# Kernel optimization log

Measured on AMD Instinct MI355X. Metric: run time of the kernel, lower is better.

Reference implementation:

```python
import jax, jax.numpy as jnp
import numpy as np

B, A, N_IN = 128, 96, 128  # molecules, atoms per molecule, feature dim
H1, H2 = 64, 1             # gated-equivariant MLP widths: 128 -> 64 -> 1


def _mlp(x, W1, b1, W2, b2):
    return jax.nn.silu(x @ W1 + b1) @ W2 + b2


def _gated_block(s, v, Wmix, Ws1, bs1, Ws2, bs2, n_out, sact):
    # s: [N, n_sin], v: [N, 3, n_vin]
    vmix = jnp.einsum('ndi,io->ndo', v, Wmix)          # [N, 3, 2*n_out]
    vV, vW = vmix[..., :n_out], vmix[..., n_out:]
    vVn = jnp.linalg.norm(vV, axis=-2)                 # [N, n_out]
    x = _mlp(jnp.concatenate([s, vVn], axis=-1), Ws1, bs1, Ws2, bs2)
    s_out, gate = x[..., :n_out], x[..., n_out:]
    v_out = gate[:, None, :] * vW                      # [N, 3, n_out]
    if sact:
        s_out = jax.nn.silu(s_out)
    return s_out, v_out


def setup_inputs():
    key = jax.random.key(0)
    ks = iter(jax.random.split(key, 40))
    def W(shape):
        return jax.random.normal(next(ks), shape, jnp.float32) / np.sqrt(shape[0]).astype(np.float32)
    N = B * A
    return dict(
        positions=jax.random.normal(next(ks), (N, 3), jnp.float32) * 3.0,
        scalar_rep=jax.random.normal(next(ks), (N, N_IN), jnp.float32),
        vector_rep=jax.random.normal(next(ks), (N, 3, N_IN), jnp.float32),
        mix_W1=W((N_IN, 2 * H1)),
        sc1_W1=W((N_IN + H1, N_IN)), sc1_b1=jnp.zeros((N_IN,), jnp.float32),
        sc1_W2=W((N_IN, 2 * H1)), sc1_b2=jnp.zeros((2 * H1,), jnp.float32),
        mix_W2=W((H1, 2 * H2)),
        sc2_W1=W((H1 + H2, H1)), sc2_b1=jnp.zeros((H1,), jnp.float32),
        sc2_W2=W((H1, 2 * H2)), sc2_b2=jnp.zeros((2 * H2,), jnp.float32),
        vv_W1=W((9, 30)), vv_b1=jnp.zeros((30,), jnp.float32), vv_W2=W((30, 9)), vv_b2=jnp.zeros((9,), jnp.float32),
        vr_W1=W((9, 30)), vr_b1=jnp.zeros((30,), jnp.float32), vr_W2=W((30, 9)), vr_b2=jnp.zeros((9,), jnp.float32),
        s_W1=W((2, 30)), s_b1=jnp.zeros((30,), jnp.float32), s_W2=W((30, 9)), s_b2=jnp.zeros((9,), jnp.float32),
        h_W1=W((9, 30)), h_b1=jnp.zeros((30,), jnp.float32), h_W2=W((30, 9)), h_b2=jnp.zeros((9,), jnp.float32),
        n_atoms=jnp.full((B,), A, dtype=jnp.int32),
    )


def reference(positions, scalar_rep, vector_rep,
              mix_W1, sc1_W1, sc1_b1, sc1_W2, sc1_b2,
              mix_W2, sc2_W1, sc2_b1, sc2_W2, sc2_b2,
              vv_W1, vv_b1, vv_W2, vv_b2,
              vr_W1, vr_b1, vr_W2, vr_b2,
              s_W1, s_b1, s_W2, s_b2,
              h_W1, h_b1, h_W2, h_b2, n_atoms):
    # outnet: gated equivariant MLP 128 -> 64 (silu on scalars) -> 1 (no sact)
    s, v = _gated_block(scalar_rep, vector_rep, mix_W1, sc1_W1, sc1_b1, sc1_W2, sc1_b2, H1, True)
    s, v = _gated_block(s, v, mix_W2, sc2_W1, sc2_b1, sc2_W2, sc2_b2, H2, False)
    l0 = s[:, 0].reshape(B, A)          # [B, A]
    l1 = v[:, :, 0].reshape(B, A, 3)    # [B, A, 3]
    pos = positions.reshape(B, A, 3)
    # per-pair outer products, flattened 3x3 -> 9 (row-major k,l as in torch view)
    vv = jnp.einsum('bik,bjl->bijkl', l1, l1).reshape(B, A, A, 9)
    vr = jnp.einsum('bik,bjl->bijkl', l1, pos).reshape(B, A, A, 9)
    vv = _mlp(vv, vv_W1, vv_b1, vv_W2, vv_b2)
    vr = _mlp(vr, vr_W1, vr_b1, vr_W2, vr_b2)
    sp = jnp.stack([jnp.broadcast_to(l0[:, :, None], (B, A, A)),
                    jnp.broadcast_to(l0[:, None, :], (B, A, A))], axis=-1)  # [B,A,A,2] = (s_i, s_j)
    sp = _mlp(sp, s_W1, s_b1, s_W2, s_b2)
    h = _mlp(vv + vr + sp, h_W1, h_b1, h_W2, h_b2).reshape(B, A, A, 3, 3)
    # permute(0,2,1,3) per molecule -> block Hessian [3A, 3A]
    h = jnp.transpose(h, (0, 1, 3, 2, 4)).reshape(B, 3 * A, 3 * A)
    return h.reshape(-1, 27)
```

## Files before the change

### kernel.cpp

```cpp
#include <hip/hip_runtime.h>
#include <cstddef>

#define A_ATOMS 96
#define BATCH   128
#define NNODES  12288
#define NB      8
#define AS      132
#define XS      196

typedef float v2f __attribute__((ext_vector_type(2)));

__device__ __forceinline__ float silu_f(float x) {
    float e = __expf(-x);
    return x * __builtin_amdgcn_rcpf(1.0f + e);
}
__device__ __forceinline__ v2f silu2(v2f x) {
    v2f r; r.x = silu_f(x.x); r.y = silu_f(x.y); return r;
}

#define RED64(v) { v += __shfl_xor(v, 1); v += __shfl_xor(v, 2); v += __shfl_xor(v, 4); \
                   v += __shfl_xor(v, 8); v += __shfl_xor(v, 16); v += __shfl_xor(v, 32); }
#define RED16(v) { v += __shfl_xor(v, 1); v += __shfl_xor(v, 2); v += __shfl_xor(v, 4); \
                   v += __shfl_xor(v, 8); }

__global__ __launch_bounds__(256)
void node_k(const float* __restrict__ vrep, const float* __restrict__ mixW1,
            const float* __restrict__ srep,
            const float* __restrict__ sc1W1, const float* __restrict__ sc1b1,
            const float* __restrict__ sc1W2, const float* __restrict__ sc1b2,
            const float* __restrict__ mixW2,
            const float* __restrict__ sc2W1, const float* __restrict__ sc2b1,
            const float* __restrict__ sc2W2, const float* __restrict__ sc2b2,
            float* __restrict__ l0v, float* __restrict__ l1v) {
    __shared__ float AsL[24 * AS];
    __shared__ float xinS[NB * XS];
    __shared__ float s1s[4][64];
    __shared__ float vn2s[NB];
    __shared__ float pw2s[NB][3];

    const int t  = threadIdx.x;
    const int tx = t & 31;
    const int ty = t >> 5;
    const int row0  = blockIdx.x * 24;
    const int node0 = blockIdx.x * NB;

#pragma unroll
    for (int it = 0; it < 3; it++) {
        const int idx = it * 256 + t;
        const int r   = idx >> 5;
        const int c4  = (idx & 31) * 4;
        *(float4*)&AsL[r * AS + c4] = *(const float4*)(vrep + (size_t)(row0 + r) * 128 + c4);
    }
    {
        const int a  = t >> 5;
        const int c4 = (t & 31) * 4;
        *(float4*)&xinS[a * XS + c4] = *(const float4*)(srep + (size_t)(node0 + a) * 128 + c4);
    }
    __syncthreads();

    float acc[3][4];
#pragma unroll
    for (int i = 0; i < 3; i++)
#pragma unroll
        for (int j = 0; j < 4; j++) acc[i][j] = 0.0f;

    for (int kc = 0; kc < 128; kc += 8) {
        float a0[8], a1[8], a2[8];
        *(float4*)&a0[0] = *(const float4*)&AsL[(3 * ty + 0) * AS + kc];
        *(float4*)&a0[4] = *(const float4*)&AsL[(3 * ty + 0) * AS + kc + 4];
        *(float4*)&a1[0] = *(const float4*)&AsL[(3 * ty + 1) * AS + kc];
        *(float4*)&a1[4] = *(const float4*)&AsL[(3 * ty + 1) * AS + kc + 4];
        *(float4*)&a2[0] = *(const float4*)&AsL[(3 * ty + 2) * AS + kc];
        *(float4*)&a2[4] = *(const float4*)&AsL[(3 * ty + 2) * AS + kc + 4];
#pragma unroll
        for (int kk = 0; kk < 8; kk++) {
            float b[4];
            *(float4*)b = *(const float4*)(mixW1 + (size_t)(kc + kk) * 128 + tx * 4);
#pragma unroll
            for (int j = 0; j < 4; j++) {
                acc[0][j] += a0[kk] * b[j];
                acc[1][j] += a1[kk] * b[j];
                acc[2][j] += a2[kk] * b[j];
            }
        }
    }
    if (tx < 16) {
        float nrm[4];
#pragma unroll
        for (int c = 0; c < 4; c++)
            nrm[c] = sqrtf(acc[0][c] * acc[0][c] + acc[1][c] * acc[1][c]
                         + acc[2][c] * acc[2][c]);
        *(float4*)&xinS[ty * XS + 128 + tx * 4] = *(float4*)nrm;
    }
    __syncthreads();

    float* workS = AsL;
    {
        float acc3[4];
#pragma unroll
        for (int j = 0; j < 4; j++) acc3[j] = 0.0f;
        for (int kc = 0; kc < 192; kc += 8) {
            float af[8];
            *(float4*)&af[0] = *(const float4*)&xinS[ty * XS + kc];
            *(float4*)&af[4] = *(const float4*)&xinS[ty * XS + kc + 4];
#pragma unroll
            for (int kk = 0; kk < 8; kk++) {
                float b[4];
                *(float4*)b = *(const float4*)(sc1W1 + (size_t)(kc + kk) * 128 + tx * 4);
#pragma unroll
                for (int j = 0; j < 4; j++) acc3[j] += af[kk] * b[j];
            }
        }
        float h[4];
#pragma unroll
        for (int j = 0; j < 4; j++) h[j] = silu_f(acc3[j] + sc1b1[tx * 4 + j]);
        __syncthreads();
        *(float4*)&workS[ty * AS + tx * 4] = *(float4*)h;
    }
    __syncthreads();

    float xg[4];
    {
        float acc4[4];
#pragma unroll
        for (int j = 0; j < 4; j++) acc4[j] = 0.0f;
        for (int kc = 0; kc < 128; kc += 8) {
            float af[8];
            *(float4*)&af[0] = *(const float4*)&workS[ty * AS + kc];
            *(float4*)&af[4] = *(const float4*)&workS[ty * AS + kc + 4];
#pragma unroll
            for (int kk = 0; kk < 8; kk++) {
                float b[4];
                *(float4*)b = *(const float4*)(sc1W2 + (size_t)(kc + kk) * 128 + tx * 4);
#pragma unroll
                for (int j = 0; j < 4; j++) acc4[j] += af[kk] * b[j];
            }
        }
        if (tx < 16) {
            float xs[4];
#pragma unroll
            for (int j = 0; j < 4; j++) xs[j] = acc4[j] + sc1b2[tx * 4 + j];
            *(float4*)&xinS[ty * XS + tx * 4] = *(float4*)xs;
        } else {
#pragma unroll
            for (int j = 0; j < 4; j++) xg[j] = acc4[j] + sc1b2[tx * 4 + j];
        }
    }

    if (tx >= 16) {
        const int hc = (tx - 16) * 4;
        float p0 = 0, p1 = 0, p2 = 0, p3 = 0, p4 = 0, p5 = 0;
#pragma unroll
        for (int c = 0; c < 4; c++) {
            float2 m = *(const float2*)(mixW2 + (size_t)(hc + c) * 2);
            const float v0 = xg[c] * acc[0][c];
            const float v1 = xg[c] * acc[1][c];
            const float v2 = xg[c] * acc[2][c];
            p0 += v0 * m.x; p1 += v0 * m.y;
            p2 += v1 * m.x; p3 += v1 * m.y;
            p4 += v2 * m.x; p5 += v2 * m.y;
        }
        RED16(p0); RED16(p1); RED16(p2); RED16(p3); RED16(p4); RED16(p5);
        if (tx == 16) {
            vn2s[ty] = sqrtf(p0 * p0 + p2 * p2 + p4 * p4);
            pw2s[ty][0] = p1; pw2s[ty][1] = p3; pw2s[ty][2] = p5;
        }
    }
    __syncthreads();

    {
        const int w = t >> 6, lane = t & 63;
        const float bb1 = sc2b1[lane];
        const float wn  = sc2W1[64 * 64 + lane];
        const float wq0 = sc2W2[lane * 2 + 0], wq1 = sc2W2[lane * 2 + 1];
#pragma unroll
        for (int r = 0; r < 2; r++) {
            const int nl = r * 4 + w;
            const float s1 = silu_f(xinS[nl * XS + lane]);
            s1s[w][lane] = s1;
            __builtin_amdgcn_s_waitcnt(0);
            float acc5 = bb1 + vn2s[nl] * wn;
#pragma unroll 8
            for (int i2 = 0; i2 < 64; i2++) acc5 += s1s[w][i2] * sc2W1[i2 * 64 + lane];
            const float h2 = silu_f(acc5);
            float q0 = h2 * wq0, q1 = h2 * wq1;
            RED64(q0); RED64(q1);
            if (lane == 0) {
                const int n = node0 + nl;
                const float gate = q1 + sc2b2[1];
                l0v[n] = q0 + sc2b2[0];
                l1v[(size_t)n * 3 + 0] = gate * pw2s[nl][0];
                l1v[(size_t)n * 3 + 1] = gate * pw2s[nl][1];
                l1v[(size_t)n * 3 + 2] = gate * pw2s[nl][2];
            }
        }
    }
}

__global__ __launch_bounds__(256)
void pairpre_k(const float* __restrict__ l1v, const float* __restrict__ pos,
               const float* __restrict__ l0v,
               const float* __restrict__ vvW1, const float* __restrict__ vrW1,
               const float* __restrict__ sW1, const float* __restrict__ sb1,
               float* __restrict__ Pv, float* __restrict__ Pr,
               float* __restrict__ Ps) {
    const int jl = threadIdx.x & 31;
    const int hq = threadIdx.x >> 5;
    const int j  = blockIdx.x * 32 + jl;
    const float lj0 = l1v[j * 3 + 0], lj1 = l1v[j * 3 + 1], lj2 = l1v[j * 3 + 2];
    const float pj0 = pos[j * 3 + 0], pj1 = pos[j * 3 + 1], pj2 = pos[j * 3 + 2];
    const float l0j = l0v[j];
#pragma unroll
    for (int hh = 0; hh < 4; hh++) {
        const int h = hq * 4 + hh;
        if (h < 30) {
#pragma unroll
            for (int a = 0; a < 3; a++) {
                float v = lj0 * vvW1[(3 * a + 0) * 30 + h] + lj1 * vvW1[(3 * a + 1) * 30 + h]
                        + lj2 * vvW1[(3 * a + 2) * 30 + h];
                float r = pj0 * vrW1[(3 * a + 0) * 30 + h] + pj1 * vrW1[(3 * a + 1) * 30 + h]
                        + pj2 * vrW1[(3 * a + 2) * 30 + h];
                Pv[(size_t)(a * 30 + h) * NNODES + j] = v;
                Pr[(size_t)(a * 30 + h) * NNODES + j] = r;
            }
            Ps[(size_t)h * NNODES + j] = sb1[h] + l0j * sW1[30 + h];
        }
    }
}

__global__ __launch_bounds__(192)
void pair_k(const float* __restrict__ l0v, const float* __restrict__ l1v,
            const float* __restrict__ Pv, const float* __restrict__ Pr,
            const float* __restrict__ Ps,
            const float* __restrict__ vvb1, const float* __restrict__ vrb1,
            const float* __restrict__ sW1,
            const float* __restrict__ vvW2, const float* __restrict__ vrW2,
            const float* __restrict__ sW2,
            const float* __restrict__ vvb2, const float* __restrict__ vrb2,
            const float* __restrict__ sb2,
            const float* __restrict__ hW1,  const float* __restrict__ hb1,
            const float* __restrict__ hW2,  const float* __restrict__ hb2,
            float* __restrict__ out) {
    const int t = threadIdx.x;
    const int b = blockIdx.y;
    const int g = (t >= 96) ? 1 : 0;
    const int j = t - g * 96;
    const int i0 = blockIdx.x * 4 + g * 2;
    const int ni0 = b * A_ATOMS + i0;
    const int ni1 = ni0 + 1;
    const int nj  = b * A_ATOMS + j;

    const v2f li0 = { l1v[ni0 * 3 + 0], l1v[ni1 * 3 + 0] };
    const v2f li1 = { l1v[ni0 * 3 + 1], l1v[ni1 * 3 + 1] };
    const v2f li2 = { l1v[ni0 * 3 + 2], l1v[ni1 * 3 + 2] };
    const v2f s0i = { l0v[ni0], l0v[ni1] };

    v2f t9[9];
#pragma unroll
    for (int l = 0; l < 9; l++) t9[l] = (v2f)(vvb2[l] + vrb2[l] + sb2[l]);

    for (int h = 0; h < 30; h++) {
        const float pv0 = Pv[(size_t)h * NNODES + nj];
        const float pv1 = Pv[(size_t)(30 + h) * NNODES + nj];
        const float pv2 = Pv[(size_t)(60 + h) * NNODES + nj];
        const float pr0 = Pr[(size_t)h * NNODES + nj];
        const float pr1 = Pr[(size_t)(30 + h) * NNODES + nj];
        const float pr2 = Pr[(size_t)(60 + h) * NNODES + nj];
        const float ps  = Ps[(size_t)h * NNODES + nj];

        v2f av = (v2f)(vvb1[h]) + li0 * pv0 + li1 * pv1 + li2 * pv2;
        v2f ar = (v2f)(vrb1[h]) + li0 * pr0 + li1 * pr1 + li2 * pr2;
        v2f as = (v2f)(ps) + s0i * sW1[h];
        av = silu2(av); ar = silu2(ar); as = silu2(as);
#pragma unroll
        for (int l = 0; l < 9; l++)
            t9[l] += av * vvW2[h * 9 + l] + ar * vrW2[h * 9 + l] + as * sW2[h * 9 + l];
    }

    v2f o9[9];
#pragma unroll
    for (int l = 0; l < 9; l++) o9[l] = (v2f)(hb2[l]);
    for (int h = 0; h < 30; h++) {
        v2f a = (v2f)(hb1[h]);
#pragma unroll
        for (int m = 0; m < 9; m++) a += t9[m] * hW1[m * 30 + h];
        a = silu2(a);
#pragma unroll
        for (int l = 0; l < 9; l++) o9[l] += a * hW2[h * 9 + l];
    }

    const size_t rb0 = (size_t)ni0;
#pragma unroll
    for (int k = 0; k < 3; k++) {
        const size_t off0 = (rb0 * 3 + k) * 288 + (size_t)j * 3;
        const size_t off1 = off0 + 3 * 288;
        out[off0 + 0] = o9[3 * k + 0].x;
        out[off0 + 1] = o9[3 * k + 1].x;
        out[off0 + 2] = o9[3 * k + 2].x;
        out[off1 + 0] = o9[3 * k + 0].y;
        out[off1 + 1] = o9[3 * k + 1].y;
        out[off1 + 2] = o9[3 * k + 2].y;
    }
}

extern "C" void kernel_launch(void* const* d_in, const int* in_sizes, int n_in,
                              void* d_out, int out_size, void* d_ws, size_t ws_size,
                              hipStream_t stream) {
    const float* pos   = (const float*)d_in[0];
    const float* srep  = (const float*)d_in[1];
    const float* vrep  = (const float*)d_in[2];
    const float* mixW1 = (const float*)d_in[3];
    const float* sc1W1 = (const float*)d_in[4];
    const float* sc1b1 = (const float*)d_in[5];
    const float* sc1W2 = (const float*)d_in[6];
    const float* sc1b2 = (const float*)d_in[7];
    const float* mixW2 = (const float*)d_in[8];
    const float* sc2W1 = (const float*)d_in[9];
    const float* sc2b1 = (const float*)d_in[10];
    const float* sc2W2 = (const float*)d_in[11];
    const float* sc2b2 = (const float*)d_in[12];
    const float* vvW1  = (const float*)d_in[13];
    const float* vvb1  = (const float*)d_in[14];
    const float* vvW2  = (const float*)d_in[15];
    const float* vvb2  = (const float*)d_in[16];
    const float* vrW1  = (const float*)d_in[17];
    const float* vrb1  = (const float*)d_in[18];
    const float* vrW2  = (const float*)d_in[19];
    const float* vrb2  = (const float*)d_in[20];
    const float* sW1   = (const float*)d_in[21];
    const float* sb1   = (const float*)d_in[22];
    const float* sW2   = (const float*)d_in[23];
    const float* sb2   = (const float*)d_in[24];
    const float* hW1   = (const float*)d_in[25];
    const float* hb1   = (const float*)d_in[26];
    const float* hW2   = (const float*)d_in[27];
    const float* hb2   = (const float*)d_in[28];

    float* ws  = (float*)d_ws;
    float* Pv  = ws;
    float* Pr  = Pv + 1105920;
    float* Ps  = Pr + 1105920;
    float* l0v = Ps + 368640;
    float* l1v = l0v + 12288;
    float* outf = (float*)d_out;

    node_k<<<NNODES / NB, 256, 0, stream>>>(
        vrep, mixW1, srep,
        sc1W1, sc1b1, sc1W2, sc1b2,
        mixW2, sc2W1, sc2b1, sc2W2, sc2b2,
        l0v, l1v);

    pairpre_k<<<NNODES / 32, 256, 0, stream>>>(l1v, pos, l0v, vvW1, vrW1,
                                               sW1, sb1, Pv, Pr, Ps);

    pair_k<<<dim3(A_ATOMS / 4, BATCH), 192, 0, stream>>>(
        l0v, l1v, Pv, Pr, Ps,
        vvb1, vrb1, sW1,
        vvW2, vrW2, sW2,
        vvb2, vrb2, sb2,
        hW1, hb1, hW2, hb2,
        outf);
}
```

Measured before the change: 298.4 us.

## Interleave pair precompute buffers, use packed FMA, halve node kernel threads

Three separate changes. The pair precompute outputs are packed into one interleaved array of 8 floats per (h, node), so pair_k reads two float4s per hidden unit instead of seven scattered scalar loads. The pair MLP arithmetic is written as explicit packed FMAs on 2-wide vectors, aiming for v_pk_fma use. node_k drops to 128 threads with 8 output columns per thread, doubling per-thread register work and reducing occupancy, in exchange for fewer threads and shorter reductions. The interleaved buffer also carries one padding float per entry.

```diff
diff --git a/kernel.cpp b/kernel.cpp
--- a/kernel.cpp
+++ b/kernel.cpp
@@ -20,10 +20,9 @@
 
 #define RED64(v) { v += __shfl_xor(v, 1); v += __shfl_xor(v, 2); v += __shfl_xor(v, 4); \
                    v += __shfl_xor(v, 8); v += __shfl_xor(v, 16); v += __shfl_xor(v, 32); }
-#define RED16(v) { v += __shfl_xor(v, 1); v += __shfl_xor(v, 2); v += __shfl_xor(v, 4); \
-                   v += __shfl_xor(v, 8); }
-
-__global__ __launch_bounds__(256)
+#define RED8(v)  { v += __shfl_xor(v, 1); v += __shfl_xor(v, 2); v += __shfl_xor(v, 4); }
+
+__global__ __launch_bounds__(128)
 void node_k(const float* __restrict__ vrep, const float* __restrict__ mixW1,
             const float* __restrict__ srep,
             const float* __restrict__ sc1W1, const float* __restrict__ sc1b1,
@@ -34,35 +33,37 @@
             float* __restrict__ l0v, float* __restrict__ l1v) {
     __shared__ float AsL[24 * AS];
     __shared__ float xinS[NB * XS];
-    __shared__ float s1s[4][64];
+    __shared__ float s1s[2][64];
     __shared__ float vn2s[NB];
     __shared__ float pw2s[NB][3];
 
     const int t  = threadIdx.x;
-    const int tx = t & 31;
-    const int ty = t >> 5;
+    const int tx = t & 15;
+    const int ty = t >> 4;
     const int row0  = blockIdx.x * 24;
     const int node0 = blockIdx.x * NB;
 
 #pragma unroll
-    for (int it = 0; it < 3; it++) {
-        const int idx = it * 256 + t;
+    for (int it = 0; it < 6; it++) {
+        const int idx = it * 128 + t;
         const int r   = idx >> 5;
         const int c4  = (idx & 31) * 4;
         *(float4*)&AsL[r * AS + c4] = *(const float4*)(vrep + (size_t)(row0 + r) * 128 + c4);
     }
-    {
-        const int a  = t >> 5;
-        const int c4 = (t & 31) * 4;
+#pragma unroll
+    for (int it = 0; it < 2; it++) {
+        const int idx = it * 128 + t;
+        const int a   = idx >> 5;
+        const int c4  = (idx & 31) * 4;
         *(float4*)&xinS[a * XS + c4] = *(const float4*)(srep + (size_t)(node0 + a) * 128 + c4);
     }
     __syncthreads();
 
-    float acc[3][4];
+    float acc[3][8];
 #pragma unroll
     for (int i = 0; i < 3; i++)
 #pragma unroll
-        for (int j = 0; j < 4; j++) acc[i][j] = 0.0f;
+        for (int j = 0; j < 8; j++) acc[i][j] = 0.0f;
 
     for (int kc = 0; kc < 128; kc += 8) {
         float a0[8], a1[8], a2[8];
@@ -74,85 +75,89 @@
         *(float4*)&a2[4] = *(const float4*)&AsL[(3 * ty + 2) * AS + kc + 4];
 #pragma unroll
         for (int kk = 0; kk < 8; kk++) {
-            float b[4];
-            *(float4*)b = *(const float4*)(mixW1 + (size_t)(kc + kk) * 128 + tx * 4);
-#pragma unroll
-            for (int j = 0; j < 4; j++) {
+            float b[8];
+            *(float4*)&b[0] = *(const float4*)(mixW1 + (size_t)(kc + kk) * 128 + tx * 8);
+            *(float4*)&b[4] = *(const float4*)(mixW1 + (size_t)(kc + kk) * 128 + tx * 8 + 4);
+#pragma unroll
+            for (int j = 0; j < 8; j++) {
                 acc[0][j] += a0[kk] * b[j];
                 acc[1][j] += a1[kk] * b[j];
                 acc[2][j] += a2[kk] * b[j];
             }
         }
     }
-    if (tx < 16) {
-        float nrm[4];
-#pragma unroll
-        for (int c = 0; c < 4; c++)
+    if (tx < 8) {
+        float nrm[8];
+#pragma unroll
+        for (int c = 0; c < 8; c++)
             nrm[c] = sqrtf(acc[0][c] * acc[0][c] + acc[1][c] * acc[1][c]
                          + acc[2][c] * acc[2][c]);
-        *(float4*)&xinS[ty * XS + 128 + tx * 4] = *(float4*)nrm;
+        *(float4*)&xinS[ty * XS + 128 + tx * 8]     = *(float4*)&nrm[0];
+        *(float4*)&xinS[ty * XS + 128 + tx * 8 + 4] = *(float4*)&nrm[4];
     }
     __syncthreads();
 
     float* workS = AsL;
     {
-        float acc3[4];
-#pragma unroll
-        for (int j = 0; j < 4; j++) acc3[j] = 0.0f;
+        float acc3[8];
+#pragma unroll
+        for (int j = 0; j < 8; j++) acc3[j] = 0.0f;
         for (int kc = 0; kc < 192; kc += 8) {
             float af[8];
             *(float4*)&af[0] = *(const float4*)&xinS[ty * XS + kc];
             *(float4*)&af[4] = *(const float4*)&xinS[ty * XS + kc + 4];
 #pragma unroll
             for (int kk = 0; kk < 8; kk++) {
-                float b[4];
-                *(float4*)b = *(const float4*)(sc1W1 + (size_t)(kc + kk) * 128 + tx * 4);
-#pragma unroll
-                for (int j = 0; j < 4; j++) acc3[j] += af[kk] * b[j];
-            }
-        }
-        float h[4];
-#pragma unroll
-        for (int j = 0; j < 4; j++) h[j] = silu_f(acc3[j] + sc1b1[tx * 4 + j]);
-        __syncthreads();
-        *(float4*)&workS[ty * AS + tx * 4] = *(float4*)h;
+                float b[8];
+                *(float4*)&b[0] = *(const float4*)(sc1W1 + (size_t)(kc + kk) * 128 + tx * 8);
+                *(float4*)&b[4] = *(const float4*)(sc1W1 + (size_t)(kc + kk) * 128 + tx * 8 + 4);
+#pragma unroll
+                for (int j = 0; j < 8; j++) acc3[j] += af[kk] * b[j];
+            }
+        }
+        float h[8];
+#pragma unroll
+        for (int j = 0; j < 8; j++) h[j] = silu_f(acc3[j] + sc1b1[tx * 8 + j]);
+        *(float4*)&workS[ty * AS + tx * 8]     = *(float4*)&h[0];
+        *(float4*)&workS[ty * AS + tx * 8 + 4] = *(float4*)&h[4];
     }
     __syncthreads();
 
-    float xg[4];
+    float xg[8];
     {
-        float acc4[4];
-#pragma unroll
-        for (int j = 0; j < 4; j++) acc4[j] = 0.0f;
+        float acc4[8];
+#pragma unroll
+        for (int j = 0; j < 8; j++) acc4[j] = 0.0f;
         for (int kc = 0; kc < 128; kc += 8) {
             float af[8];
             *(float4*)&af[0] = *(const float4*)&workS[ty * AS + kc];
             *(float4*)&af[4] = *(const float4*)&workS[ty * AS + kc + 4];
 #pragma unroll
             for (int kk = 0; kk < 8; kk++) {
-                float b[4];
-                *(float4*)b = *(const float4*)(sc1W2 + (size_t)(kc + kk) * 128 + tx * 4);
-#pragma unroll
-                for (int j = 0; j < 4; j++) acc4[j] += af[kk] * b[j];
-            }
-        }
-        if (tx < 16) {
-            float xs[4];
-#pragma unroll
-            for (int j = 0; j < 4; j++) xs[j] = acc4[j] + sc1b2[tx * 4 + j];
-            *(float4*)&xinS[ty * XS + tx * 4] = *(float4*)xs;
+                float b[8];
+                *(float4*)&b[0] = *(const float4*)(sc1W2 + (size_t)(kc + kk) * 128 + tx * 8);
+                *(float4*)&b[4] = *(const float4*)(sc1W2 + (size_t)(kc + kk) * 128 + tx * 8 + 4);
+#pragma unroll
+                for (int j = 0; j < 8; j++) acc4[j] += af[kk] * b[j];
+            }
+        }
+        if (tx < 8) {
+            float xs[8];
+#pragma unroll
+            for (int j = 0; j < 8; j++) xs[j] = acc4[j] + sc1b2[tx * 8 + j];
+            *(float4*)&xinS[ty * XS + tx * 8]     = *(float4*)&xs[0];
+            *(float4*)&xinS[ty * XS + tx * 8 + 4] = *(float4*)&xs[4];
         } else {
 #pragma unroll
-            for (int j = 0; j < 4; j++) xg[j] = acc4[j] + sc1b2[tx * 4 + j];
-        }
-    }
-
-    if (tx >= 16) {
-        const int hc = (tx - 16) * 4;
+            for (int j = 0; j < 8; j++) xg[j] = acc4[j] + sc1b2[tx * 8 + j];
+        }
+    }
+
+    if (tx >= 8) {
         float p0 = 0, p1 = 0, p2 = 0, p3 = 0, p4 = 0, p5 = 0;
 #pragma unroll
-        for (int c = 0; c < 4; c++) {
-            float2 m = *(const float2*)(mixW2 + (size_t)(hc + c) * 2);
+        for (int c = 0; c < 8; c++) {
+            float2 m = *(const float2*)(mixW2 + (size_t)((tx - 8) * 8 + c) * 2);
             const float v0 = xg[c] * acc[0][c];
             const float v1 = xg[c] * acc[1][c];
             const float v2 = xg[c] * acc[2][c];
@@ -160,8 +165,8 @@
             p2 += v1 * m.x; p3 += v1 * m.y;
             p4 += v2 * m.x; p5 += v2 * m.y;
         }
-        RED16(p0); RED16(p1); RED16(p2); RED16(p3); RED16(p4); RED16(p5);
-        if (tx == 16) {
+        RED8(p0); RED8(p1); RED8(p2); RED8(p3); RED8(p4); RED8(p5);
+        if (tx == 8) {
             vn2s[ty] = sqrtf(p0 * p0 + p2 * p2 + p4 * p4);
             pw2s[ty][0] = p1; pw2s[ty][1] = p3; pw2s[ty][2] = p5;
         }
@@ -174,8 +179,8 @@
         const float wn  = sc2W1[64 * 64 + lane];
         const float wq0 = sc2W2[lane * 2 + 0], wq1 = sc2W2[lane * 2 + 1];
 #pragma unroll
-        for (int r = 0; r < 2; r++) {
-            const int nl = r * 4 + w;
+        for (int r = 0; r < 4; r++) {
+            const int nl = r * 2 + w;
             const float s1 = silu_f(xinS[nl * XS + lane]);
             s1s[w][lane] = s1;
             __builtin_amdgcn_s_waitcnt(0);
@@ -202,8 +207,7 @@
                const float* __restrict__ l0v,
                const float* __restrict__ vvW1, const float* __restrict__ vrW1,
                const float* __restrict__ sW1, const float* __restrict__ sb1,
-               float* __restrict__ Pv, float* __restrict__ Pr,
-               float* __restrict__ Ps) {
+               float* __restrict__ PT) {
     const int jl = threadIdx.x & 31;
     const int hq = threadIdx.x >> 5;
     const int j  = blockIdx.x * 32 + jl;
@@ -214,24 +218,29 @@
     for (int hh = 0; hh < 4; hh++) {
         const int h = hq * 4 + hh;
         if (h < 30) {
+            float pv[3], pr[3];
 #pragma unroll
             for (int a = 0; a < 3; a++) {
-                float v = lj0 * vvW1[(3 * a + 0) * 30 + h] + lj1 * vvW1[(3 * a + 1) * 30 + h]
-                        + lj2 * vvW1[(3 * a + 2) * 30 + h];
-                float r = pj0 * vrW1[(3 * a + 0) * 30 + h] + pj1 * vrW1[(3 * a + 1) * 30 + h]
-                        + pj2 * vrW1[(3 * a + 2) * 30 + h];
-                Pv[(size_t)(a * 30 + h) * NNODES + j] = v;
-                Pr[(size_t)(a * 30 + h) * NNODES + j] = r;
-            }
-            Ps[(size_t)h * NNODES + j] = sb1[h] + l0j * sW1[30 + h];
-        }
-    }
-}
+                pv[a] = lj0 * vvW1[(3 * a + 0) * 30 + h] + lj1 * vvW1[(3 * a + 1) * 30 + h]
+                      + lj2 * vvW1[(3 * a + 2) * 30 + h];
+                pr[a] = pj0 * vrW1[(3 * a + 0) * 30 + h] + pj1 * vrW1[(3 * a + 1) * 30 + h]
+                      + pj2 * vrW1[(3 * a + 2) * 30 + h];
+            }
+            const float ps = sb1[h] + l0j * sW1[30 + h];
+            float4 q0 = { pv[0], pv[1], pv[2], pr[0] };
+            float4 q1 = { pr[1], pr[2], ps, 0.0f };
+            float* p = PT + ((size_t)h * NNODES + j) * 8;
+            *(float4*)p       = q0;
+            *(float4*)(p + 4) = q1;
+        }
+    }
+}
+
+#define PKFMA(a, b, c) __builtin_elementwise_fma((a), (b), (c))
 
 __global__ __launch_bounds__(192)
 void pair_k(const float* __restrict__ l0v, const float* __restrict__ l1v,
-            const float* __restrict__ Pv, const float* __restrict__ Pr,
-            const float* __restrict__ Ps,
+            const float* __restrict__ PT,
             const float* __restrict__ vvb1, const float* __restrict__ vrb1,
             const float* __restrict__ sW1,
             const float* __restrict__ vvW2, const float* __restrict__ vrW2,
@@ -259,22 +268,23 @@
 #pragma unroll
     for (int l = 0; l < 9; l++) t9[l] = (v2f)(vvb2[l] + vrb2[l] + sb2[l]);
 
+    const float* pt = PT + (size_t)nj * 8;
     for (int h = 0; h < 30; h++) {
-        const float pv0 = Pv[(size_t)h * NNODES + nj];
-        const float pv1 = Pv[(size_t)(30 + h) * NNODES + nj];
-        const float pv2 = Pv[(size_t)(60 + h) * NNODES + nj];
-        const float pr0 = Pr[(size_t)h * NNODES + nj];
-        const float pr1 = Pr[(size_t)(30 + h) * NNODES + nj];
-        const float pr2 = Pr[(size_t)(60 + h) * NNODES + nj];
-        const float ps  = Ps[(size_t)h * NNODES + nj];
-
-        v2f av = (v2f)(vvb1[h]) + li0 * pv0 + li1 * pv1 + li2 * pv2;
-        v2f ar = (v2f)(vrb1[h]) + li0 * pr0 + li1 * pr1 + li2 * pr2;
-        v2f as = (v2f)(ps) + s0i * sW1[h];
+        float4 q0 = *(const float4*)(pt + (size_t)h * NNODES * 8);
+        float4 q1 = *(const float4*)(pt + (size_t)h * NNODES * 8 + 4);
+
+        v2f av = PKFMA(li2, (v2f)(q0.z), PKFMA(li1, (v2f)(q0.y),
+                 PKFMA(li0, (v2f)(q0.x), (v2f)(vvb1[h]))));
+        v2f ar = PKFMA(li2, (v2f)(q1.y), PKFMA(li1, (v2f)(q1.x),
+                 PKFMA(li0, (v2f)(q0.w), (v2f)(vrb1[h]))));
+        v2f as = PKFMA(s0i, (v2f)(sW1[h]), (v2f)(q1.z));
         av = silu2(av); ar = silu2(ar); as = silu2(as);
 #pragma unroll
-        for (int l = 0; l < 9; l++)
-            t9[l] += av * vvW2[h * 9 + l] + ar * vrW2[h * 9 + l] + as * sW2[h * 9 + l];
+        for (int l = 0; l < 9; l++) {
+            t9[l] = PKFMA(av, (v2f)(vvW2[h * 9 + l]), t9[l]);
+            t9[l] = PKFMA(ar, (v2f)(vrW2[h * 9 + l]), t9[l]);
+            t9[l] = PKFMA(as, (v2f)(sW2[h * 9 + l]), t9[l]);
+        }
     }
 
     v2f o9[9];
@@ -283,10 +293,10 @@
     for (int h = 0; h < 30; h++) {
         v2f a = (v2f)(hb1[h]);
 #pragma unroll
-        for (int m = 0; m < 9; m++) a += t9[m] * hW1[m * 30 + h];
+        for (int m = 0; m < 9; m++) a = PKFMA(t9[m], (v2f)(hW1[m * 30 + h]), a);
         a = silu2(a);
 #pragma unroll
-        for (int l = 0; l < 9; l++) o9[l] += a * hW2[h * 9 + l];
+        for (int l = 0; l < 9; l++) o9[l] = PKFMA(a, (v2f)(hW2[h * 9 + l]), o9[l]);
     }
 
     const size_t rb0 = (size_t)ni0;
@@ -337,24 +347,22 @@
     const float* hb2   = (const float*)d_in[28];
 
     float* ws  = (float*)d_ws;
-    float* Pv  = ws;
-    float* Pr  = Pv + 1105920;
-    float* Ps  = Pr + 1105920;
-    float* l0v = Ps + 368640;
+    float* PT  = ws;
+    float* l0v = PT + 2949120;
     float* l1v = l0v + 12288;
     float* outf = (float*)d_out;
 
-    node_k<<<NNODES / NB, 256, 0, stream>>>(
+    node_k<<<NNODES / NB, 128, 0, stream>>>(
         vrep, mixW1, srep,
         sc1W1, sc1b1, sc1W2, sc1b2,
         mixW2, sc2W1, sc2b1, sc2W2, sc2b2,
         l0v, l1v);
 
     pairpre_k<<<NNODES / 32, 256, 0, stream>>>(l1v, pos, l0v, vvW1, vrW1,
-                                               sW1, sb1, Pv, Pr, Ps);
+                                               sW1, sb1, PT);
 
     pair_k<<<dim3(A_ATOMS / 4, BATCH), 192, 0, stream>>>(
-        l0v, l1v, Pv, Pr, Ps,
+        l0v, l1v, PT,
         vvb1, vrb1, sW1,
         vvW2, vrW2, sW2,
         vvb2, vrb2, sb2,
```

Measured after the change: 313.7 us. 1.05x slower.
